# Kernel optimization log

Measured on AMD Instinct MI355X. Metric: run time of the kernel, lower is better.

## Reference

```python
import jax, jax.numpy as jnp
import numpy as np

MARGIN = 0.3


def setup_inputs() -> dict:
    key = jax.random.key(0)
    k1, k2 = jax.random.split(key)
    N, D, C = 8192, 512, 1024
    embeddings = jax.random.normal(k1, (N, D), dtype=jnp.float32)
    labels = jax.random.randint(k2, (N,), 0, C, dtype=jnp.int64)
    return {"embeddings": embeddings, "labels": labels}


def reference(embeddings, labels):
    # L2-normalize rows, cosine distance via Gram matrix: d = 1 - e_i . e_j
    e = embeddings / jnp.linalg.norm(embeddings, axis=1, keepdims=True)
    dist = 1.0 - jnp.matmul(e, e.T)  # [N, N]

    same = labels[:, None] == labels[None, :]           # [N, N] bool
    eye = jnp.eye(labels.shape[0], dtype=bool)
    pos_mask = same & ~eye                              # positives exclude self
    neg_mask = ~same                                    # negatives

    # Batch-hard mining: hardest (farthest) positive, hardest (closest) negative
    hardest_pos = jnp.max(jnp.where(pos_mask, dist, -jnp.inf), axis=1)
    hardest_neg = jnp.min(jnp.where(neg_mask, dist, jnp.inf), axis=1)

    loss = jax.nn.relu(hardest_pos - hardest_neg + MARGIN)
    return jnp.mean(loss)
```

## Files before the change

kernel.cpp:

```cpp
#include <hip/hip_runtime.h>
#include <hip/hip_fp8.h>
#include <hip/hip_fp16.h>
#include <stdint.h>

#define MARGIN 0.3f

constexpr int N = 8192;
constexpr int D = 512;
constexpr int BM = 128, BN = 128;
constexpr int NKB = D / 32;
constexpr int NT = N / BM;
constexpr int NPAIR = NT * (NT + 1) / 2;
constexpr int WEDGE = NPAIR / 8;
constexpr float ESCALE = 16.0f;
constexpr float INV_SC2 = 1.0f / (ESCALE * ESCALE);

typedef float f32x4 __attribute__((ext_vector_type(4)));

__device__ __forceinline__ unsigned char f2fp8(float f) {
  return __hip_fp8_e4m3(f).__x;
}

__device__ __forceinline__ unsigned packMM(float mn, float mx) {
  unsigned short a = __half_as_ushort(__float2half(mn));
  unsigned short b = __half_as_ushort(__float2half(mx));
  return (unsigned)a | ((unsigned)b << 16);
}
__device__ __forceinline__ float unpLo(unsigned u) {
  return __half2float(__ushort_as_half((unsigned short)(u & 0xffff)));
}
__device__ __forceinline__ float unpHi(unsigned u) {
  return __half2float(__ushort_as_half((unsigned short)(u >> 16)));
}
__device__ __forceinline__ unsigned combMM(unsigned A, unsigned B) {
  return packMM(fminf(unpLo(A), unpLo(B)), fmaxf(unpHi(A), unpHi(B)));
}

__device__ __forceinline__ void pair_from_q(int q, int& ti, int& tj) {
  int SI = 0;
  while (32 * (SI + 1) * (SI + 1) + 4 * (SI + 1) <= q) ++SI;
  int r = q - (32 * SI * SI + 4 * SI);
  int i, j, SJ;
  if (r < 64 * SI) {
    SJ = r >> 6;
    int w = r & 63;
    i = w >> 3;
    j = w & 7;
  } else {
    int d = r - 64 * SI;
    SJ = SI;
    i = 0;
    while ((i + 1) * (i + 2) / 2 <= d) ++i;
    j = d - i * (i + 1) / 2;
  }
  ti = SI * 8 + i;
  tj = SJ * 8 + j;
}


__global__ __launch_bounds__(256) void normalize_rows(
    const float* __restrict__ emb, unsigned char* __restrict__ e8,
    float* __restrict__ out) {
  if (blockIdx.x == 0 && threadIdx.x == 0) out[0] = 0.f;
  const int wave = threadIdx.x >> 6, lane = threadIdx.x & 63;
  const int row = blockIdx.x * 4 + wave;
  const float4* src = (const float4*)(emb + (size_t)row * D);
  float4 x0 = src[lane];
  float4 x1 = src[lane + 64];
  float ss = x0.x * x0.x + x0.y * x0.y + x0.z * x0.z + x0.w * x0.w +
             x1.x * x1.x + x1.y * x1.y + x1.z * x1.z + x1.w * x1.w;
#pragma unroll
  for (int m = 1; m < 64; m <<= 1) ss += __shfl_xor(ss, m, 64);
  const float r = rsqrtf(ss) * ESCALE;
  union { unsigned char b[8]; uint2 u; } o;
  o.b[0] = f2fp8(x0.x * r); o.b[1] = f2fp8(x0.y * r);
  o.b[2] = f2fp8(x0.z * r); o.b[3] = f2fp8(x0.w * r);
  o.b[4] = f2fp8(x1.x * r); o.b[5] = f2fp8(x1.y * r);
  o.b[6] = f2fp8(x1.z * r); o.b[7] = f2fp8(x1.w * r);
  const unsigned off = (unsigned)(row >> 4) * 8192 + (unsigned)(lane >> 2) * 512 +
                       (row & 15) * 32 + (lane & 3) * 8;
  *(uint2*)(e8 + off) = o.u;
}

__global__ __launch_bounds__(256, 3) void bh_gemm_sym(
    const unsigned char* __restrict__ e8, const int* __restrict__ labels,
    unsigned* __restrict__ scr) {
  __shared__ unsigned bufR[2][128];
  __shared__ unsigned bufC[2][128];

  const int b = blockIdx.x;
  const int q = WEDGE * (b & 7) + (b >> 3);
  int ti, tj;
  pair_from_q(q, ti, tj);
  const int iBase = ti * BM, jBase = tj * BN;
  const bool diag = (ti == tj);

  const int tid = threadIdx.x;
  const int lane = tid & 63;
  const int wave = tid >> 6;
  const int wr = wave >> 1, wc = wave & 1;
  const int quad = lane >> 4, n16 = lane & 15;

  const unsigned laneOff = (unsigned)n16 * 32 + (unsigned)quad * 8;
  const unsigned char* aP[4];
  const unsigned char* bP[4];
#pragma unroll
  for (int r = 0; r < 4; ++r) {
    aP[r] = e8 + (unsigned)(iBase + wr * 64 + r * 16) * 512 + laneOff;
    bP[r] = e8 + (unsigned)(jBase + wc * 64 + r * 16) * 512 + laneOff;
  }

  f32x4 acc[4][4];
#pragma unroll
  for (int r = 0; r < 4; ++r)
#pragma unroll
    for (int c = 0; c < 4; ++c) acc[r][c] = (f32x4)0.0f;

  long abuf[4][4], bbuf[4][4];
#pragma unroll
  for (int ph = 0; ph < 3; ++ph)
#pragma unroll
    for (int r = 0; r < 4; ++r) {
      abuf[ph][r] = *(const long*)(aP[r] + ph * 512);
      bbuf[ph][r] = *(const long*)(bP[r] + ph * 512);
    }

#pragma unroll
  for (int kb = 0; kb < NKB; ++kb) {
    const int cur = kb & 3;
    if (kb + 3 < NKB) {
      const int nxt = (kb + 3) & 3;
#pragma unroll
      for (int r = 0; r < 4; ++r) {
        abuf[nxt][r] = *(const long*)(aP[r] + (kb + 3) * 512);
        bbuf[nxt][r] = *(const long*)(bP[r] + (kb + 3) * 512);
      }
    }
#pragma unroll
    for (int r = 0; r < 4; ++r)
#pragma unroll
      for (int c = 0; c < 4; ++c)
        acc[r][c] = __builtin_amdgcn_mfma_f32_16x16x32_fp8_fp8(
            abuf[cur][r], bbuf[cur][c], acc[r][c], 0, 0, 0);
  }

  int lj[4];
#pragma unroll
  for (int c = 0; c < 4; ++c) lj[c] = labels[jBase + wc * 64 + c * 16 + n16];

  float cminp[4], cmaxn[4];
#pragma unroll
  for (int c = 0; c < 4; ++c) {
    cminp[c] = __builtin_inff();
    cmaxn[c] = -__builtin_inff();
  }

#pragma unroll
  for (int r = 0; r < 4; ++r) {
    const int rbase = wr * 64 + r * 16 + quad * 4;
    int4 li = *(const int4*)(labels + iBase + rbase);
    const int* lav = (const int*)&li;
    float minp[4], maxn[4];
#pragma unroll
    for (int v = 0; v < 4; ++v) {
      minp[v] = __builtin_inff();
      maxn[v] = -__builtin_inff();
    }
#pragma unroll
    for (int c = 0; c < 4; ++c) {
      const int col_ = wc * 64 + c * 16 + n16;
#pragma unroll
      for (int v = 0; v < 4; ++v) {
        float s = acc[r][c][v] * INV_SC2;
        bool same = (lav[v] == lj[c]);
        float pv = same ? s : __builtin_inff();
        float nv = same ? -__builtin_inff() : s;
        if (diag && (rbase + v) == col_) pv = __builtin_inff();
        minp[v] = fminf(minp[v], pv);
        maxn[v] = fmaxf(maxn[v], nv);
        cminp[c] = fminf(cminp[c], same ? s : __builtin_inff());
        cmaxn[c] = fmaxf(cmaxn[c], same ? -__builtin_inff() : s);
      }
    }
#pragma unroll
    for (int m = 1; m <= 8; m <<= 1) {
#pragma unroll
      for (int v = 0; v < 4; ++v) {
        minp[v] = fminf(minp[v], __shfl_xor(minp[v], m, 64));
        maxn[v] = fmaxf(maxn[v], __shfl_xor(maxn[v], m, 64));
      }
    }
    if (n16 == 0) {
#pragma unroll
      for (int v = 0; v < 4; ++v)
        bufR[wc][rbase + v] = packMM(minp[v], maxn[v]);
    }
  }

  if (!diag) {
#pragma unroll
    for (int m = 16; m <= 32; m <<= 1) {
#pragma unroll
      for (int c = 0; c < 4; ++c) {
        cminp[c] = fminf(cminp[c], __shfl_xor(cminp[c], m, 64));
        cmaxn[c] = fmaxf(cmaxn[c], __shfl_xor(cmaxn[c], m, 64));
      }
    }
    if (quad == 0) {
#pragma unroll
      for (int c = 0; c < 4; ++c)
        bufC[wr][wc * 64 + c * 16 + n16] = packMM(cminp[c], cmaxn[c]);
    }
  }

  __syncthreads();

  if (wc == 0) {
    const int row = wr * 64 + lane;
    scr[(unsigned)(iBase + row) * 64 + tj] = combMM(bufR[0][row], bufR[1][row]);
  }
  if (!diag && wr == 0) {
    const int col = wc * 64 + lane;
    scr[(unsigned)(jBase + col) * 64 + ti] = combMM(bufC[0][col], bufC[1][col]);
  }
}

__global__ __launch_bounds__(256) void finalize_loss(
    const unsigned* __restrict__ scr, float* __restrict__ out) {
  const int row = blockIdx.x * 256 + threadIdx.x;
  const uint4* p = (const uint4*)(scr + (unsigned)row * 64);
  float mn = __builtin_inff(), mx = -__builtin_inff();
#pragma unroll
  for (int i = 0; i < 16; ++i) {
    uint4 w = p[i];
    mn = fminf(fminf(fminf(mn, unpLo(w.x)), unpLo(w.y)), fminf(unpLo(w.z), unpLo(w.w)));
    mx = fmaxf(fmaxf(fmaxf(mx, unpHi(w.x)), unpHi(w.y)), fmaxf(unpHi(w.z), unpHi(w.w)));
  }
  float loss = mx - mn + MARGIN;
  float sum = loss > 0.f ? loss : 0.f;
#pragma unroll
  for (int m = 1; m < 64; m <<= 1) sum += __shfl_xor(sum, m, 64);
  __shared__ float ws4[4];
  const int lane = threadIdx.x & 63, wave = threadIdx.x >> 6;
  if (lane == 0) ws4[wave] = sum;
  __syncthreads();
  if (threadIdx.x == 0)
    atomicAdd(out, (ws4[0] + ws4[1] + ws4[2] + ws4[3]) * (1.0f / N));
}

extern "C" void kernel_launch(void* const* d_in, const int* in_sizes, int n_in,
                              void* d_out, int out_size, void* d_ws, size_t ws_size,
                              hipStream_t stream) {
  const float* emb = (const float*)d_in[0];
  const int* labels = (const int*)d_in[1];
  float* out = (float*)d_out;

  unsigned char* e8 = (unsigned char*)d_ws;
  unsigned* scr = (unsigned*)((char*)d_ws + (size_t)4 * 1024 * 1024);

  normalize_rows<<<N / 4, 256, 0, stream>>>(emb, e8, out);
  bh_gemm_sym<<<NPAIR, 256, 0, stream>>>(e8, labels, scr);
  finalize_loss<<<N / 256, 256, 0, stream>>>(scr, out);
}
```

Before: 114.2 us.

## Use 32x32x64 scaled FP8 MFMA with LDS staging and packed-f16 min reductions

Swaps the 16x16x32 FP8 MFMA for the larger 32x32x64 scaled f8f6f4 MFMA. Operand tiles are now staged through double-buffered LDS using global_load_lds, with a swizzled e8 layout written by the normalize kernel to avoid bank conflicts. The epilogue packs (s, -s) into a single f16x2 word with cvt_pkrtz and reduces with v_pk_min_f16, using a transpose-style shuffle tree in place of separate float min and max passes. This aims to cut MFMA issue count and epilogue ALU/shuffle work, at the cost of extra LDS traffic, barriers and tighter f16 range and rounding.

After: 102.6 us. 1.11x faster.

```diff
diff --git a/kernel.cpp b/kernel.cpp
--- a/kernel.cpp
+++ b/kernel.cpp
@@ -8,32 +8,33 @@
 constexpr int N = 8192;
 constexpr int D = 512;
 constexpr int BM = 128, BN = 128;
-constexpr int NKB = D / 32;
+constexpr int NKS = D / 64;
 constexpr int NT = N / BM;
 constexpr int NPAIR = NT * (NT + 1) / 2;
 constexpr int WEDGE = NPAIR / 8;
 constexpr float ESCALE = 16.0f;
 constexpr float INV_SC2 = 1.0f / (ESCALE * ESCALE);
 
-typedef float f32x4 __attribute__((ext_vector_type(4)));
+typedef int i32x8 __attribute__((ext_vector_type(8)));
+typedef float f32x16 __attribute__((ext_vector_type(16)));
+typedef __fp16 h2 __attribute__((ext_vector_type(2)));
+
+constexpr unsigned INF2 = 0x7C007C00u;
 
 __device__ __forceinline__ unsigned char f2fp8(float f) {
   return __hip_fp8_e4m3(f).__x;
 }
 
-__device__ __forceinline__ unsigned packMM(float mn, float mx) {
-  unsigned short a = __half_as_ushort(__float2half(mn));
-  unsigned short b = __half_as_ushort(__float2half(mx));
-  return (unsigned)a | ((unsigned)b << 16);
-}
-__device__ __forceinline__ float unpLo(unsigned u) {
-  return __half2float(__ushort_as_half((unsigned short)(u & 0xffff)));
-}
-__device__ __forceinline__ float unpHi(unsigned u) {
-  return __half2float(__ushort_as_half((unsigned short)(u >> 16)));
-}
-__device__ __forceinline__ unsigned combMM(unsigned A, unsigned B) {
-  return packMM(fminf(unpLo(A), unpLo(B)), fmaxf(unpHi(A), unpHi(B)));
+__device__ __forceinline__ unsigned pkmin(unsigned a, unsigned b) {
+  unsigned d;
+  asm("v_pk_min_f16 %0, %1, %2" : "=v"(d) : "v"(a), "v"(b));
+  return d;
+}
+
+__device__ __forceinline__ unsigned cvtpk(float lo, float hi) {
+  union { h2 h; unsigned u; } cv;
+  cv.h = __builtin_amdgcn_cvt_pkrtz(lo, hi);
+  return cv.u;
 }
 
 __device__ __forceinline__ void pair_from_q(int q, int& ti, int& tj) {
@@ -77,14 +78,18 @@
   o.b[2] = f2fp8(x0.z * r); o.b[3] = f2fp8(x0.w * r);
   o.b[4] = f2fp8(x1.x * r); o.b[5] = f2fp8(x1.y * r);
   o.b[6] = f2fp8(x1.z * r); o.b[7] = f2fp8(x1.w * r);
-  const unsigned off = (unsigned)(row >> 4) * 8192 + (unsigned)(lane >> 2) * 512 +
-                       (row & 15) * 32 + (lane & 3) * 8;
+  const int n = row & 31;
+  const unsigned inner =
+      ((unsigned)(n * 64 + ((lane >> 1) & 3) * 16) ^
+       ((unsigned)((n >> 1) & 7) << 4)) + (lane & 1) * 8;
+  const unsigned off = (unsigned)((row >> 5) * 8 + (lane >> 3)) * 2048 + inner;
   *(uint2*)(e8 + off) = o.u;
 }
 
 __global__ __launch_bounds__(256, 3) void bh_gemm_sym(
     const unsigned char* __restrict__ e8, const int* __restrict__ labels,
     unsigned* __restrict__ scr) {
+  __shared__ unsigned char lds[2][16384];
   __shared__ unsigned bufR[2][128];
   __shared__ unsigned bufC[2][128];
 
@@ -99,117 +104,146 @@
   const int lane = tid & 63;
   const int wave = tid >> 6;
   const int wr = wave >> 1, wc = wave & 1;
-  const int quad = lane >> 4, n16 = lane & 15;
-
-  const unsigned laneOff = (unsigned)n16 * 32 + (unsigned)quad * 8;
-  const unsigned char* aP[4];
-  const unsigned char* bP[4];
-#pragma unroll
-  for (int r = 0; r < 4; ++r) {
-    aP[r] = e8 + (unsigned)(iBase + wr * 64 + r * 16) * 512 + laneOff;
-    bP[r] = e8 + (unsigned)(jBase + wc * 64 + r * 16) * 512 + laneOff;
-  }
-
-  f32x4 acc[4][4];
-#pragma unroll
-  for (int r = 0; r < 4; ++r)
-#pragma unroll
-    for (int c = 0; c < 4; ++c) acc[r][c] = (f32x4)0.0f;
-
-  long abuf[4][4], bbuf[4][4];
-#pragma unroll
-  for (int ph = 0; ph < 3; ++ph)
-#pragma unroll
-    for (int r = 0; r < 4; ++r) {
-      abuf[ph][r] = *(const long*)(aP[r] + ph * 512);
-      bbuf[ph][r] = *(const long*)(bP[r] + ph * 512);
-    }
-
-#pragma unroll
-  for (int kb = 0; kb < NKB; ++kb) {
-    const int cur = kb & 3;
-    if (kb + 3 < NKB) {
-      const int nxt = (kb + 3) & 3;
-#pragma unroll
-      for (int r = 0; r < 4; ++r) {
-        abuf[nxt][r] = *(const long*)(aP[r] + (kb + 3) * 512);
-        bbuf[nxt][r] = *(const long*)(bP[r] + (kb + 3) * 512);
+  const int n = lane & 31, hi = lane >> 5;
+
+  const unsigned o0 =
+      (unsigned)(n * 64 + hi * 32) ^ ((unsigned)((n >> 1) & 7) << 4);
+
+  const unsigned char* gsrc[4];
+  unsigned ldst[4];
+#pragma unroll
+  for (int j = 0; j < 4; ++j) {
+    const int id = wave * 4 + j;
+    const int mat = id >> 3;
+    const int fb = (id & 7) >> 1;
+    const int rb = (mat ? (jBase >> 5) : (iBase >> 5)) + fb;
+    gsrc[j] = e8 + (size_t)(rb * 8) * 2048 + (id & 1) * 1024 + lane * 16;
+    ldst[j] = (unsigned)id * 1024 + lane * 16;
+  }
+
+  auto STAGE = [&](int T, int buf) {
+#pragma unroll
+    for (int j = 0; j < 4; ++j)
+      __builtin_amdgcn_global_load_lds(
+          (const __attribute__((address_space(1))) unsigned int*)(gsrc[j] +
+                                                                  (size_t)T * 2048),
+          (__attribute__((address_space(3))) unsigned int*)(&lds[buf][ldst[j]]),
+          16, 0, 0);
+  };
+
+  f32x16 acc[2][2];
+#pragma unroll
+  for (int t = 0; t < 2; ++t)
+#pragma unroll
+    for (int c = 0; c < 2; ++c) acc[t][c] = (f32x16)0.0f;
+
+  STAGE(0, 0);
+  __syncthreads();
+#pragma unroll
+  for (int T = 0; T < NKS; ++T) {
+    const int cur = T & 1;
+    if (T + 1 < NKS) STAGE(T + 1, cur ^ 1);
+    union { i32x8 v; int4 q2[2]; } aF[2], bF[2];
+#pragma unroll
+    for (int t = 0; t < 2; ++t) {
+      const unsigned char* ab = &lds[cur][(wr * 2 + t) * 2048];
+      aF[t].q2[0] = *(const int4*)(ab + o0);
+      aF[t].q2[1] = *(const int4*)(ab + (o0 ^ 16));
+      const unsigned char* bb = &lds[cur][8192 + (wc * 2 + t) * 2048];
+      bF[t].q2[0] = *(const int4*)(bb + o0);
+      bF[t].q2[1] = *(const int4*)(bb + (o0 ^ 16));
+    }
+#pragma unroll
+    for (int t = 0; t < 2; ++t)
+#pragma unroll
+      for (int c = 0; c < 2; ++c)
+        acc[t][c] = __builtin_amdgcn_mfma_scale_f32_32x32x64_f8f6f4(
+            aF[t].v, bF[c].v, acc[t][c], 0, 0,
+            0, 127, 0, 127);
+    __syncthreads();
+  }
+
+  int lj[2];
+#pragma unroll
+  for (int c = 0; c < 2; ++c) lj[c] = labels[jBase + wc * 64 + c * 32 + n];
+
+  unsigned colAcc[2] = {INF2, INF2};
+
+#pragma unroll
+  for (int t = 0; t < 2; ++t) {
+    int li[16];
+#pragma unroll
+    for (int a = 0; a < 4; ++a) {
+      int4 v = *(const int4*)(labels + iBase + wr * 64 + t * 32 + 4 * hi + 8 * a);
+      li[4 * a + 0] = v.x; li[4 * a + 1] = v.y;
+      li[4 * a + 2] = v.z; li[4 * a + 3] = v.w;
+    }
+    unsigned P[2][16];
+#pragma unroll
+    for (int c = 0; c < 2; ++c) {
+#pragma unroll
+      for (int r = 0; r < 16; ++r) {
+        const float s = acc[t][c][r];
+        const unsigned u = cvtpk(s, -s);
+        const bool same = (li[r] == lj[c]);
+        const unsigned sel = same ? 0x0000FFFFu : 0xFFFF0000u;
+        unsigned p = (sel & u) | (~sel & INF2);
+        if (diag) {
+          const int row32 = (r & 3) + 8 * (r >> 2) + 4 * hi;
+          const bool self =
+              (wr * 64 + t * 32 + row32) == (wc * 64 + c * 32 + n);
+          p = self ? INF2 : p;
+        }
+        P[c][r] = p;
       }
-    }
-#pragma unroll
-    for (int r = 0; r < 4; ++r)
-#pragma unroll
-      for (int c = 0; c < 4; ++c)
-        acc[r][c] = __builtin_amdgcn_mfma_f32_16x16x32_fp8_fp8(
-            abuf[cur][r], bbuf[cur][c], acc[r][c], 0, 0, 0);
-  }
-
-  int lj[4];
-#pragma unroll
-  for (int c = 0; c < 4; ++c) lj[c] = labels[jBase + wc * 64 + c * 16 + n16];
-
-  float cminp[4], cmaxn[4];
-#pragma unroll
-  for (int c = 0; c < 4; ++c) {
-    cminp[c] = __builtin_inff();
-    cmaxn[c] = -__builtin_inff();
-  }
-
-#pragma unroll
-  for (int r = 0; r < 4; ++r) {
-    const int rbase = wr * 64 + r * 16 + quad * 4;
-    int4 li = *(const int4*)(labels + iBase + rbase);
-    const int* lav = (const int*)&li;
-    float minp[4], maxn[4];
-#pragma unroll
-    for (int v = 0; v < 4; ++v) {
-      minp[v] = __builtin_inff();
-      maxn[v] = -__builtin_inff();
-    }
-#pragma unroll
-    for (int c = 0; c < 4; ++c) {
-      const int col_ = wc * 64 + c * 16 + n16;
-#pragma unroll
-      for (int v = 0; v < 4; ++v) {
-        float s = acc[r][c][v] * INV_SC2;
-        bool same = (lav[v] == lj[c]);
-        float pv = same ? s : __builtin_inff();
-        float nv = same ? -__builtin_inff() : s;
-        if (diag && (rbase + v) == col_) pv = __builtin_inff();
-        minp[v] = fminf(minp[v], pv);
-        maxn[v] = fmaxf(maxn[v], nv);
-        cminp[c] = fminf(cminp[c], same ? s : __builtin_inff());
-        cmaxn[c] = fmaxf(cmaxn[c], same ? -__builtin_inff() : s);
+      if (!diag) {
+        unsigned cm = P[c][0];
+#pragma unroll
+        for (int r = 1; r < 16; ++r) cm = pkmin(cm, P[c][r]);
+        colAcc[c] = pkmin(colAcc[c], cm);
       }
     }
-#pragma unroll
-    for (int m = 1; m <= 8; m <<= 1) {
-#pragma unroll
-      for (int v = 0; v < 4; ++v) {
-        minp[v] = fminf(minp[v], __shfl_xor(minp[v], m, 64));
-        maxn[v] = fmaxf(maxn[v], __shfl_xor(maxn[v], m, 64));
-      }
-    }
-    if (n16 == 0) {
-#pragma unroll
-      for (int v = 0; v < 4; ++v)
-        bufR[wc][rbase + v] = packMM(minp[v], maxn[v]);
-    }
+    unsigned m[16];
+#pragma unroll
+    for (int r = 0; r < 16; ++r) m[r] = pkmin(P[0][r], P[1][r]);
+    unsigned w8[8];
+#pragma unroll
+    for (int i = 0; i < 8; ++i) {
+      unsigned x = pkmin(m[2 * i],     __shfl_xor(m[2 * i],     16, 64));
+      unsigned y = pkmin(m[2 * i + 1], __shfl_xor(m[2 * i + 1], 16, 64));
+      w8[i] = (lane & 16) ? y : x;
+    }
+    unsigned w4[4];
+#pragma unroll
+    for (int i = 0; i < 4; ++i) {
+      unsigned x = pkmin(w8[2 * i],     __shfl_xor(w8[2 * i],     8, 64));
+      unsigned y = pkmin(w8[2 * i + 1], __shfl_xor(w8[2 * i + 1], 8, 64));
+      w4[i] = (lane & 8) ? y : x;
+    }
+    unsigned w2[2];
+#pragma unroll
+    for (int i = 0; i < 2; ++i) {
+      unsigned x = pkmin(w4[2 * i],     __shfl_xor(w4[2 * i],     4, 64));
+      unsigned y = pkmin(w4[2 * i + 1], __shfl_xor(w4[2 * i + 1], 4, 64));
+      w2[i] = (lane & 4) ? y : x;
+    }
+    unsigned x1 = pkmin(w2[0], __shfl_xor(w2[0], 2, 64));
+    unsigned y1 = pkmin(w2[1], __shfl_xor(w2[1], 2, 64));
+    unsigned w1 = (lane & 2) ? y1 : x1;
+    w1 = pkmin(w1, __shfl_xor(w1, 1, 64));
+    const int row32 = 16 * ((lane >> 1) & 1) + 8 * ((lane >> 2) & 1) + 4 * hi +
+                      2 * ((lane >> 3) & 1) + ((lane >> 4) & 1);
+    if ((lane & 1) == 0) bufR[wc][wr * 64 + t * 32 + row32] = w1;
   }
 
   if (!diag) {
 #pragma unroll
-    for (int m = 16; m <= 32; m <<= 1) {
-#pragma unroll
-      for (int c = 0; c < 4; ++c) {
-        cminp[c] = fminf(cminp[c], __shfl_xor(cminp[c], m, 64));
-        cmaxn[c] = fmaxf(cmaxn[c], __shfl_xor(cmaxn[c], m, 64));
-      }
-    }
-    if (quad == 0) {
-#pragma unroll
-      for (int c = 0; c < 4; ++c)
-        bufC[wr][wc * 64 + c * 16 + n16] = packMM(cminp[c], cmaxn[c]);
+    for (int c = 0; c < 2; ++c)
+      colAcc[c] = pkmin(colAcc[c], __shfl_xor(colAcc[c], 32, 64));
+    if (hi == 0) {
+#pragma unroll
+      for (int c = 0; c < 2; ++c)
+        bufC[wr][wc * 64 + c * 32 + n] = colAcc[c];
     }
   }
 
@@ -217,26 +251,27 @@
 
   if (wc == 0) {
     const int row = wr * 64 + lane;
-    scr[(unsigned)(iBase + row) * 64 + tj] = combMM(bufR[0][row], bufR[1][row]);
+    scr[(unsigned)(iBase + row) * 64 + tj] = pkmin(bufR[0][row], bufR[1][row]);
   }
   if (!diag && wr == 0) {
     const int col = wc * 64 + lane;
-    scr[(unsigned)(jBase + col) * 64 + ti] = combMM(bufC[0][col], bufC[1][col]);
+    scr[(unsigned)(jBase + col) * 64 + ti] = pkmin(bufC[0][col], bufC[1][col]);
   }
 }
 
 __global__ __launch_bounds__(256) void finalize_loss(
     const unsigned* __restrict__ scr, float* __restrict__ out) {
   const int row = blockIdx.x * 256 + threadIdx.x;
-  const uint4* p = (const uint4*)(scr + (unsigned)row * 64);
-  float mn = __builtin_inff(), mx = -__builtin_inff();
+  const uint4* p = (const uint4*)(scr + (size_t)row * 64);
+  unsigned mm = INF2;
 #pragma unroll
   for (int i = 0; i < 16; ++i) {
     uint4 w = p[i];
-    mn = fminf(fminf(fminf(mn, unpLo(w.x)), unpLo(w.y)), fminf(unpLo(w.z), unpLo(w.w)));
-    mx = fmaxf(fmaxf(fmaxf(mx, unpHi(w.x)), unpHi(w.y)), fmaxf(unpHi(w.z), unpHi(w.w)));
-  }
-  float loss = mx - mn + MARGIN;
+    mm = pkmin(mm, pkmin(pkmin(w.x, w.y), pkmin(w.z, w.w)));
+  }
+  const float mn = __half2float(__ushort_as_half((unsigned short)(mm & 0xffff)));
+  const float nmx = __half2float(__ushort_as_half((unsigned short)(mm >> 16)));
+  float loss = (-nmx - mn) * INV_SC2 + MARGIN;
   float sum = loss > 0.f ? loss : 0.f;
 #pragma unroll
   for (int m = 1; m < 64; m <<= 1) sum += __shfl_xor(sum, m, 64);
```
